# Kernel optimization log

Measured on AMD Instinct MI355X. Metric: run time of the kernel, lower is better.

The kernel has to match this reference:

```python
import jax, jax.numpy as jnp
import numpy as np

NUM_INPUTS = 8
NUM_MFS = 3
NUM_RULES = NUM_MFS ** NUM_INPUTS  # 6561
BATCH = 8192


def setup_inputs() -> dict:
    key = jax.random.key(0)
    k1, k2, k3 = jax.random.split(key, 3)
    x = jax.random.normal(k1, (BATCH, NUM_INPUTS), dtype=jnp.float32)
    # one GaussianMF per input: centers ~ randn(num_mfs)
    centers = jax.random.normal(k2, (NUM_INPUTS, NUM_MFS), dtype=jnp.float32)
    # sigmas fixed buffer [0.3, 0.5, 0.7] shared across all inputs
    sigmas = jnp.array([0.3, 0.5, 0.7], dtype=jnp.float32)
    consequents = jax.random.normal(k3, (NUM_RULES, NUM_INPUTS + 1), dtype=jnp.float32)
    return {"x": x, "centers": centers, "sigmas": sigmas, "consequents": consequents}


def reference(x, centers, sigmas, consequents):
    B, nI = x.shape
    M = centers.shape[1]
    # Gaussian memberships: [B, nI, M]
    mu = jnp.exp(-0.5 * ((x[:, :, None] - centers[None, :, :]) / sigmas[None, None, :]) ** 2)
    # Rule strengths via successive outer products (lexicographic order matches
    # itertools.product(range(M), repeat=nI): first input varies slowest).
    s = mu[:, 0, :]  # [B, M]
    for j in range(1, nI):
        s = (s[:, :, None] * mu[:, j, None, :]).reshape(B, -1)  # [B, M^(j+1)]
    # s: [B, NUM_RULES]
    ones = jnp.ones((B, 1), dtype=x.dtype)
    xb = jnp.concatenate([x, ones], axis=1)  # [B, nI+1]
    rule_outputs = jnp.einsum('bi,ri->br', xb, consequents)  # [B, R]
    out = jnp.sum(s * rule_outputs, axis=1) / (jnp.sum(s, axis=1) + 1e-6)
    return out[:, None]
```

## Files before the change

### kernel.cpp

```cpp
#include <hip/hip_runtime.h>
#include <math.h>

#define BATCH   8192
#define NI      8
#define NM      3
#define NR      6561
#define NROWS   81
#define NL      81

__device__ __forceinline__ float sel3(const float* a, int i) {
    return (i == 0) ? a[0] : ((i == 1) ? a[1] : a[2]);
}

__global__ __launch_bounds__(256, 8) void sugeno_partial(
    const float* __restrict__ x,
    const float* __restrict__ centers,
    const float* __restrict__ sigmas,
    const float* __restrict__ cons,
    float* __restrict__ partial,
    int nchunk)
{
    const int b     = blockIdx.x * 256 + threadIdx.x;
    const int chunk = blockIdx.y;

    const float4* xv = reinterpret_cast<const float4*>(x + (size_t)b * NI);
    float4 xa = xv[0], xb4 = xv[1];
    float xr[NI];
    xr[0]=xa.x; xr[1]=xa.y; xr[2]=xa.z; xr[3]=xa.w;
    xr[4]=xb4.x; xr[5]=xb4.y; xr[6]=xb4.z; xr[7]=xb4.w;

    float inv[NM];
    #pragma unroll
    for (int m = 0; m < NM; ++m) {
        float s = sigmas[m];
        inv[m] = -0.5f / (s * s);
    }

    float mu[NI][NM];
    #pragma unroll
    for (int j = 0; j < NI; ++j) {
        #pragma unroll
        for (int m = 0; m < NM; ++m) {
            float d = xr[j] - centers[j * NM + m];
            mu[j][m] = __expf(d * d * inv[m]);
        }
    }

    const int rH0 = (chunk * NROWS) / nchunk;
    const int rH1 = ((chunk + 1) * NROWS) / nchunk;

    float V[9];
    #pragma unroll
    for (int i = 0; i < 9; ++i) V[i] = 0.0f;

    for (int rH = rH0; rH < rH1; ++rH) {
        int d0 = rH / 27, rem = rH - d0 * 27;
        int d1 = rem / 9;  rem -= d1 * 9;
        int d2 = rem / 3;
        int d3 = rem - d2 * 3;
        const float ph = sel3(mu[0], d0) * sel3(mu[1], d1)
                       * sel3(mu[2], d2) * sel3(mu[3], d3);
        const float* __restrict__ crow = cons + (size_t)rH * NL * 9;

        #pragma unroll
        for (int m4 = 0; m4 < 3; ++m4) {
            const float p4 = ph * mu[4][m4];
            #pragma unroll
            for (int m5 = 0; m5 < 3; ++m5) {
                const float p5 = p4 * mu[5][m5];
                #pragma unroll
                for (int m6 = 0; m6 < 3; ++m6) {
                    const float p6 = p5 * mu[6][m6];
                    #pragma unroll
                    for (int m7 = 0; m7 < 3; ++m7) {
                        const float s = p6 * mu[7][m7];
                        const float* cr = crow + (size_t)((((m4*3+m5)*3+m6)*3)+m7) * 9;
                        #pragma unroll
                        for (int i = 0; i < 9; ++i) V[i] += s * cr[i];
                    }
                }
            }
        }
    }

    const float numer = V[0]*xr[0] + V[1]*xr[1] + V[2]*xr[2] + V[3]*xr[3]
                      + V[4]*xr[4] + V[5]*xr[5] + V[6]*xr[6] + V[7]*xr[7]
                      + V[8];
    partial[(size_t)chunk * BATCH + b] = numer;
}

__global__ __launch_bounds__(256) void sugeno_reduce(
    const float* __restrict__ x,
    const float* __restrict__ centers,
    const float* __restrict__ sigmas,
    const float* __restrict__ partial,
    float* __restrict__ out,
    int nchunk)
{
    const int b = blockIdx.x * blockDim.x + threadIdx.x;
    if (b >= BATCH) return;

    const float4* xv = reinterpret_cast<const float4*>(x + (size_t)b * NI);
    float4 xa = xv[0], xb4 = xv[1];
    float xr[NI];
    xr[0]=xa.x; xr[1]=xa.y; xr[2]=xa.z; xr[3]=xa.w;
    xr[4]=xb4.x; xr[5]=xb4.y; xr[6]=xb4.z; xr[7]=xb4.w;

    float inv[NM];
    #pragma unroll
    for (int m = 0; m < NM; ++m) {
        float s = sigmas[m];
        inv[m] = -0.5f / (s * s);
    }

    float denom = 1.0f;
    #pragma unroll
    for (int j = 0; j < NI; ++j) {
        float srow = 0.0f;
        #pragma unroll
        for (int m = 0; m < NM; ++m) {
            float d = xr[j] - centers[j * NM + m];
            srow += __expf(d * d * inv[m]);
        }
        denom *= srow;
    }

    float numer = 0.0f;
    #pragma unroll 4
    for (int k = 0; k < nchunk; ++k)
        numer += partial[(size_t)k * BATCH + b];

    out[b] = numer / (denom + 1e-6f);
}

extern "C" void kernel_launch(void* const* d_in, const int* in_sizes, int n_in,
                              void* d_out, int out_size, void* d_ws, size_t ws_size,
                              hipStream_t stream)
{
    const float* x       = (const float*)d_in[0];
    const float* centers = (const float*)d_in[1];
    const float* sigmas  = (const float*)d_in[2];
    const float* cons    = (const float*)d_in[3];
    float* out           = (float*)d_out;
    float* partial       = (float*)d_ws;

    int nchunk = (int)(ws_size / ((size_t)BATCH * sizeof(float)));
    if (nchunk > NROWS) nchunk = NROWS;
    if (nchunk < 1)     nchunk = 1;

    dim3 grid1(BATCH / 256, nchunk, 1);
    sugeno_partial<<<grid1, dim3(256, 1, 1), 0, stream>>>(x, centers, sigmas, cons,
                                                          partial, nchunk);

    dim3 grid2(BATCH / 256, 1, 1);
    sugeno_reduce<<<grid2, dim3(256, 1, 1), 0, stream>>>(x, centers, sigmas,
                                                         partial, out, nchunk);
}
```

Before: 27.87 us.

## Pack consequents to fp16 pairs and use dot2 with max-shifted exponentials

Adds a prep kernel that converts the consequents to packed fp16 pairs. The main kernel then uses v_dot2 fp32-accumulate instructions over pairs of rules and hard-codes one block row per rH. Memberships are computed with exp2 after subtracting each input's maximum exponent, so the fp16 rule strengths stay in range, and the reduce kernel restores the scale with exp2(Ksum). The reduce kernel is also restructured as a 4-wave split over rows with a shared-memory combine. This aims to halve both the FMA count and the consequent bandwidth, at the cost of fp16 precision in the weights and strengths, an extra launch, and a larger workspace requirement that is no longer checked against ws_size.

```diff
diff --git a/kernel.cpp b/kernel.cpp
--- a/kernel.cpp
+++ b/kernel.cpp
@@ -1,27 +1,67 @@
 #include <hip/hip_runtime.h>
 #include <math.h>
+#include <stdint.h>
 
 #define BATCH   8192
 #define NI      8
 #define NM      3
-#define NR      6561
 #define NROWS   81
 #define NL      81
+#define NPAIR   41
+#define HROW    (NPAIR * 9)
+#define IL2C    (-0.72134752f)
+
+typedef uint32_t u32;
+typedef __fp16 h2 __attribute__((ext_vector_type(2)));
+
+__device__ __forceinline__ h2 pack_h2(float a, float b) {
+#if __has_builtin(__builtin_amdgcn_cvt_pkrtz)
+    return __builtin_amdgcn_cvt_pkrtz(a, b);
+#else
+    h2 r; r.x = (__fp16)a; r.y = (__fp16)b; return r;
+#endif
+}
+
+__device__ __forceinline__ float fdot2(h2 a, h2 b, float c) {
+#if __has_builtin(__builtin_amdgcn_fdot2)
+    return __builtin_amdgcn_fdot2(a, b, c, false);
+#else
+    return c + (float)a.x * (float)b.x + (float)a.y * (float)b.y;
+#endif
+}
+
+__device__ __forceinline__ h2 as_h2(u32 v) { return __builtin_bit_cast(h2, v); }
 
 __device__ __forceinline__ float sel3(const float* a, int i) {
     return (i == 0) ? a[0] : ((i == 1) ? a[1] : a[2]);
 }
 
-__global__ __launch_bounds__(256, 8) void sugeno_partial(
+__global__ __launch_bounds__(256) void sugeno_prep(
+    const float* __restrict__ cons,
+    u32* __restrict__ H)
+{
+    int t = blockIdx.x * 256 + threadIdx.x;
+    if (t >= NROWS * HROW) return;
+    int rH  = t / HROW;
+    int rem = t - rH * HROW;
+    int p   = rem / 9;
+    int i   = rem - p * 9;
+    int rl0 = 2 * p, rl1 = 2 * p + 1;
+    float c0 = cons[(size_t)(rH * NL + rl0) * 9 + i];
+    float c1 = (rl1 < NL) ? cons[(size_t)(rH * NL + rl1) * 9 + i] : 0.0f;
+    h2 hv; hv.x = (__fp16)c0; hv.y = (__fp16)c1;
+    H[t] = __builtin_bit_cast(u32, hv);
+}
+
+__global__ __launch_bounds__(256, 4) void sugeno_partial(
     const float* __restrict__ x,
     const float* __restrict__ centers,
     const float* __restrict__ sigmas,
-    const float* __restrict__ cons,
-    float* __restrict__ partial,
-    int nchunk)
-{
-    const int b     = blockIdx.x * 256 + threadIdx.x;
-    const int chunk = blockIdx.y;
+    const u32*   __restrict__ H,
+    float* __restrict__ partial)
+{
+    const int b  = blockIdx.x * 256 + threadIdx.x;
+    const int rH = blockIdx.y;
 
     const float4* xv = reinterpret_cast<const float4*>(x + (size_t)b * NI);
     float4 xa = xv[0], xb4 = xv[1];
@@ -29,64 +69,85 @@
     xr[0]=xa.x; xr[1]=xa.y; xr[2]=xa.z; xr[3]=xa.w;
     xr[4]=xb4.x; xr[5]=xb4.y; xr[6]=xb4.z; xr[7]=xb4.w;
 
-    float inv[NM];
+    float il2[NM];
     #pragma unroll
     for (int m = 0; m < NM; ++m) {
         float s = sigmas[m];
-        inv[m] = -0.5f / (s * s);
-    }
-
-    float mu[NI][NM];
+        il2[m] = IL2C / (s * s);
+    }
+
+    float a[NI][NM];
     #pragma unroll
     for (int j = 0; j < NI; ++j) {
         #pragma unroll
         for (int m = 0; m < NM; ++m) {
             float d = xr[j] - centers[j * NM + m];
-            mu[j][m] = __expf(d * d * inv[m]);
+            a[j][m] = d * d * il2[m];
         }
     }
-
-    const int rH0 = (chunk * NROWS) / nchunk;
-    const int rH1 = ((chunk + 1) * NROWS) / nchunk;
+    float K[NI];
+    #pragma unroll
+    for (int j = 0; j < NI; ++j)
+        K[j] = fmaxf(fmaxf(a[j][0], a[j][1]), a[j][2]);
+
+    const int d0 = rH / 27;
+    const int d1 = (rH / 9) % 3;
+    const int d2 = (rH / 3) % 3;
+    const int d3 = rH % 3;
+
+    float argh = (sel3(a[0], d0) - K[0]) + (sel3(a[1], d1) - K[1])
+               + (sel3(a[2], d2) - K[2]) + (sel3(a[3], d3) - K[3]);
+    float ph = exp2f(argh);
+
+    float mu4[NM], mu5[NM], mu6[NM], mu7[NM];
+    #pragma unroll
+    for (int m = 0; m < NM; ++m) {
+        mu4[m] = exp2f(a[4][m] - K[4]);
+        mu5[m] = exp2f(a[5][m] - K[5]);
+        mu6[m] = exp2f(a[6][m] - K[6]);
+        mu7[m] = exp2f(a[7][m] - K[7]);
+    }
+
+    float m45[9];
+    #pragma unroll
+    for (int p = 0; p < 3; ++p) {
+        float pa = ph * mu4[p];
+        #pragma unroll
+        for (int q = 0; q < 3; ++q) m45[p * 3 + q] = pa * mu5[q];
+    }
+    float t27[27];
+    #pragma unroll
+    for (int q = 0; q < 27; ++q)
+        t27[q] = m45[q / 3] * mu6[q % 3];
+
+    const u32* __restrict__ Hrow = H + (size_t)rH * HROW;
 
     float V[9];
     #pragma unroll
     for (int i = 0; i < 9; ++i) V[i] = 0.0f;
 
-    for (int rH = rH0; rH < rH1; ++rH) {
-        int d0 = rH / 27, rem = rH - d0 * 27;
-        int d1 = rem / 9;  rem -= d1 * 9;
-        int d2 = rem / 3;
-        int d3 = rem - d2 * 3;
-        const float ph = sel3(mu[0], d0) * sel3(mu[1], d1)
-                       * sel3(mu[2], d2) * sel3(mu[3], d3);
-        const float* __restrict__ crow = cons + (size_t)rH * NL * 9;
-
-        #pragma unroll
-        for (int m4 = 0; m4 < 3; ++m4) {
-            const float p4 = ph * mu[4][m4];
-            #pragma unroll
-            for (int m5 = 0; m5 < 3; ++m5) {
-                const float p5 = p4 * mu[5][m5];
-                #pragma unroll
-                for (int m6 = 0; m6 < 3; ++m6) {
-                    const float p6 = p5 * mu[6][m6];
-                    #pragma unroll
-                    for (int m7 = 0; m7 < 3; ++m7) {
-                        const float s = p6 * mu[7][m7];
-                        const float* cr = crow + (size_t)((((m4*3+m5)*3+m6)*3)+m7) * 9;
-                        #pragma unroll
-                        for (int i = 0; i < 9; ++i) V[i] += s * cr[i];
-                    }
-                }
-            }
-        }
+    #pragma unroll
+    for (int k = 0; k < NPAIR - 1; ++k) {
+        const int r0 = 2 * k, r1 = 2 * k + 1;
+        float s0 = t27[r0 / 3] * mu7[r0 % 3];
+        float s1 = t27[r1 / 3] * mu7[r1 % 3];
+        h2 sp = pack_h2(s0, s1);
+        #pragma unroll
+        for (int i = 0; i < 9; ++i)
+            V[i] = fdot2(sp, as_h2(Hrow[k * 9 + i]), V[i]);
+    }
+    {
+        float s80 = t27[26] * mu7[2];
+        h2 sp = pack_h2(s80, 0.0f);
+        #pragma unroll
+        for (int i = 0; i < 9; ++i)
+            V[i] = fdot2(sp, as_h2(Hrow[(NPAIR - 1) * 9 + i]), V[i]);
     }
 
     const float numer = V[0]*xr[0] + V[1]*xr[1] + V[2]*xr[2] + V[3]*xr[3]
                       + V[4]*xr[4] + V[5]*xr[5] + V[6]*xr[6] + V[7]*xr[7]
                       + V[8];
-    partial[(size_t)chunk * BATCH + b] = numer;
+    partial[(size_t)rH * BATCH + b] = numer;
 }
 
 __global__ __launch_bounds__(256) void sugeno_reduce(
@@ -94,43 +155,53 @@
     const float* __restrict__ centers,
     const float* __restrict__ sigmas,
     const float* __restrict__ partial,
-    float* __restrict__ out,
-    int nchunk)
-{
-    const int b = blockIdx.x * blockDim.x + threadIdx.x;
-    if (b >= BATCH) return;
-
-    const float4* xv = reinterpret_cast<const float4*>(x + (size_t)b * NI);
-    float4 xa = xv[0], xb4 = xv[1];
-    float xr[NI];
-    xr[0]=xa.x; xr[1]=xa.y; xr[2]=xa.z; xr[3]=xa.w;
-    xr[4]=xb4.x; xr[5]=xb4.y; xr[6]=xb4.z; xr[7]=xb4.w;
-
-    float inv[NM];
-    #pragma unroll
-    for (int m = 0; m < NM; ++m) {
-        float s = sigmas[m];
-        inv[m] = -0.5f / (s * s);
-    }
-
-    float denom = 1.0f;
-    #pragma unroll
-    for (int j = 0; j < NI; ++j) {
-        float srow = 0.0f;
+    float* __restrict__ out)
+{
+    __shared__ float red[4][64];
+    const int lane = threadIdx.x & 63;
+    const int w    = threadIdx.x >> 6;
+    const int b    = blockIdx.x * 64 + lane;
+
+    float acc = 0.0f;
+    #pragma unroll 8
+    for (int k = w; k < NROWS; k += 4)
+        acc += partial[(size_t)k * BATCH + b];
+    red[w][lane] = acc;
+    __syncthreads();
+
+    if (w == 0) {
+        float numer = red[0][lane] + red[1][lane] + red[2][lane] + red[3][lane];
+
+        const float4* xv = reinterpret_cast<const float4*>(x + (size_t)b * NI);
+        float4 xa = xv[0], xb4 = xv[1];
+        float xr[NI];
+        xr[0]=xa.x; xr[1]=xa.y; xr[2]=xa.z; xr[3]=xa.w;
+        xr[4]=xb4.x; xr[5]=xb4.y; xr[6]=xb4.z; xr[7]=xb4.w;
+
+        float il2[NM];
         #pragma unroll
         for (int m = 0; m < NM; ++m) {
-            float d = xr[j] - centers[j * NM + m];
-            srow += __expf(d * d * inv[m]);
+            float s = sigmas[m];
+            il2[m] = IL2C / (s * s);
         }
-        denom *= srow;
-    }
-
-    float numer = 0.0f;
-    #pragma unroll 4
-    for (int k = 0; k < nchunk; ++k)
-        numer += partial[(size_t)k * BATCH + b];
-
-    out[b] = numer / (denom + 1e-6f);
+
+        float S = 1.0f;
+        float Ksum = 0.0f;
+        #pragma unroll
+        for (int j = 0; j < NI; ++j) {
+            float am[NM];
+            #pragma unroll
+            for (int m = 0; m < NM; ++m) {
+                float d = xr[j] - centers[j * NM + m];
+                am[m] = d * d * il2[m];
+            }
+            S *= exp2f(am[0]) + exp2f(am[1]) + exp2f(am[2]);
+            Ksum += fmaxf(fmaxf(am[0], am[1]), am[2]);
+        }
+
+        float scale = exp2f(Ksum);
+        out[b] = numer * scale / (S + 1e-6f);
+    }
 }
 
 extern "C" void kernel_launch(void* const* d_in, const int* in_sizes, int n_in,
@@ -142,17 +213,15 @@
     const float* sigmas  = (const float*)d_in[2];
     const float* cons    = (const float*)d_in[3];
     float* out           = (float*)d_out;
-    float* partial       = (float*)d_ws;
-
-    int nchunk = (int)(ws_size / ((size_t)BATCH * sizeof(float)));
-    if (nchunk > NROWS) nchunk = NROWS;
-    if (nchunk < 1)     nchunk = 1;
-
-    dim3 grid1(BATCH / 256, nchunk, 1);
-    sugeno_partial<<<grid1, dim3(256, 1, 1), 0, stream>>>(x, centers, sigmas, cons,
-                                                          partial, nchunk);
-
-    dim3 grid2(BATCH / 256, 1, 1);
-    sugeno_reduce<<<grid2, dim3(256, 1, 1), 0, stream>>>(x, centers, sigmas,
-                                                         partial, out, nchunk);
-}
+
+    float* partial = (float*)d_ws;
+    u32*   H       = (u32*)((char*)d_ws + (size_t)NROWS * BATCH * 4);
+
+    const int prep_total = NROWS * HROW;
+    sugeno_prep<<<(prep_total + 255) / 256, 256, 0, stream>>>(cons, H);
+
+    dim3 grid1(BATCH / 256, NROWS, 1);
+    sugeno_partial<<<grid1, dim3(256, 1, 1), 0, stream>>>(x, centers, sigmas, H, partial);
+
+    sugeno_reduce<<<BATCH / 64, 256, 0, stream>>>(x, centers, sigmas, partial, out);
+}
```

After: 33.66 us. +20.8%, slower.
